# Kernel tuning notes

Measured on AMD Instinct MI355X. Metric: run time of the kernel, lower is better.

Reference implementation:

```python
import jax, jax.numpy as jnp
import numpy as np

K = 3          # kernel size
PAD = 1        # padding


def _conv2d(x, w, b):
    # plain 3x3 conv, stride 1, pad 1, NCHW / OIHW
    out = jax.lax.conv_general_dilated(
        x, w, window_strides=(1, 1), padding=((PAD, PAD), (PAD, PAD)),
        dimension_numbers=('NCHW', 'OIHW', 'NCHW'))
    return out + b[None, :, None, None]


def _deform_conv2d(x, offsets, w, b):
    # torchvision deform_conv2d semantics (stride=1, dilation=1, no mask)
    B, C, H, W = x.shape
    K2 = K * K
    off = offsets.reshape(B, K2, 2, H, W)
    dy, dx = off[:, :, 0], off[:, :, 1]              # [B,K2,H,W], (y,x) order
    ki, kj = jnp.meshgrid(jnp.arange(K), jnp.arange(K), indexing='ij')
    ki = ki.reshape(K2).astype(x.dtype)
    kj = kj.reshape(K2).astype(x.dtype)
    base_y = (jnp.arange(H, dtype=x.dtype)[None, :, None] - PAD + ki[:, None, None])  # [K2,H,1]
    base_x = (jnp.arange(W, dtype=x.dtype)[None, None, :] - PAD + kj[:, None, None])  # [K2,1,W]
    py = base_y[None] + dy                            # [B,K2,H,W] sampling rows
    px = base_x[None] + dx                            # [B,K2,H,W] sampling cols

    y0 = jnp.floor(py); x0 = jnp.floor(px)
    y1 = y0 + 1.0;      x1 = x0 + 1.0
    wy1 = py - y0; wy0 = 1.0 - wy1
    wx1 = px - x0; wx0 = 1.0 - wx1

    def corner(yc, xc, wgt):
        valid = ((yc >= 0) & (yc <= H - 1) & (xc >= 0) & (xc <= W - 1))
        iy = jnp.clip(yc, 0, H - 1).astype(jnp.int32)
        ix = jnp.clip(xc, 0, W - 1).astype(jnp.int32)
        # per-batch gather: x[b][:, iy[b], ix[b]] -> [C,K2,H,W]
        vals = jax.vmap(lambda xb, iyb, ixb: xb[:, iyb, ixb])(x, iy, ix)
        return vals * (wgt * valid.astype(x.dtype))[:, None]  # [B,C,K2,H,W]

    sampled = (corner(y0, x0, wy0 * wx0) + corner(y0, x1, wy0 * wx1)
               + corner(y1, x0, wy1 * wx0) + corner(y1, x1, wy1 * wx1))
    out = jnp.einsum('bckhw,ock->bohw', sampled, w.reshape(w.shape[0], C, K2))
    return out + b[None, :, None, None]


def setup_inputs() -> dict:
    key = jax.random.key(0)
    ks = jax.random.split(key, 6)
    B, C, O, H, W = 4, 256, 256, 64, 64
    x = jax.random.normal(ks[0], (B, C, H, W), dtype=jnp.float32)
    y = jax.random.normal(ks[1], (B, C, H, W), dtype=jnp.float32)
    # offset conv predicts 2*K*K offset channels; small init keeps offsets a few px
    offset_w = jax.random.normal(ks[2], (2 * K * K, C, K, K), dtype=jnp.float32) * 0.01
    offset_b = jax.random.normal(ks[3], (2 * K * K,), dtype=jnp.float32) * 0.01
    deform_w = jax.random.normal(ks[4], (O, C, K, K), dtype=jnp.float32) * (1.0 / np.sqrt(C * K * K))
    deform_b = jax.random.normal(ks[5], (O,), dtype=jnp.float32) * 0.01
    return {"x": x, "y": y, "offset_w": offset_w, "offset_b": offset_b,
            "deform_w": deform_w, "deform_b": deform_b}


def reference(x, y, offset_w, offset_b, deform_w, deform_b):
    offsets = _conv2d(y, offset_w, offset_b)          # [B, 2*K*K, H, W]
    return _deform_conv2d(x, offsets, deform_w, deform_b)
```

## Files before the change

### kernel.cpp

```cpp
#include <hip/hip_runtime.h>
#include <hip/hip_bf16.h>
#include <stdint.h>


typedef __bf16 bf16x8 __attribute__((ext_vector_type(8)));
typedef float  f32x4  __attribute__((ext_vector_type(4)));

__device__ __forceinline__ unsigned short f2bfu(float f) {
    union { float f; unsigned u; } v; v.f = f;
    return (unsigned short)((v.u + 0x8000u) >> 16);
}
__device__ __forceinline__ float lo16(unsigned u) {
    union { unsigned u; float f; } v; v.u = u << 16; return v.f;
}
__device__ __forceinline__ float hi16(unsigned u) {
    union { unsigned u; float f; } v; v.u = u & 0xFFFF0000u; return v.f;
}
__device__ __forceinline__ unsigned cvtpk_bf16(float lo, float hi) {
    unsigned r;
    asm("v_cvt_pk_bf16_f32 %0, %1, %2" : "=v"(r) : "v"(lo), "v"(hi));
    return r;
}
__device__ __forceinline__ unsigned blend2(unsigned u0, unsigned u1, unsigned u2, unsigned u3,
                                           float4 w) {
    float lo = w.x * lo16(u0) + w.y * lo16(u1) + w.z * lo16(u2) + w.w * lo16(u3);
    float hi = w.x * hi16(u0) + w.y * hi16(u1) + w.z * hi16(u2) + w.w * hi16(u3);
    return cvtpk_bf16(lo, hi);
}

__global__ __launch_bounds__(256) void prep_kernel(
    const float* __restrict__ x, const float* __restrict__ y,
    const float* __restrict__ ow, const float* __restrict__ dw,
    unsigned short* __restrict__ xT, unsigned short* __restrict__ yT,
    unsigned short* __restrict__ Wp2, unsigned short* __restrict__ Bo)
{
    __shared__ float tile[64 * 69];
    int blk = blockIdx.x;
    int t = threadIdx.x;
    if (blk < 2048) {
        const float* src = x; unsigned short* dst = xT;
        if (blk >= 1024) { src = y; dst = yT; blk -= 1024; }
        int cq = blk & 3;
        int bh = blk >> 2;
        int w4 = t & 15, cl0 = t >> 4;
        const float* s = src + ((size_t)(bh >> 6) * 256 + cq * 64) * 4096 + (size_t)(bh & 63) * 64;
#pragma unroll
        for (int p = 0; p < 4; ++p) {
            int cl = p * 16 + cl0;
            float4 v = *(const float4*)&s[(size_t)cl * 4096 + w4 * 4];
            tile[(w4 * 4 + 0) * 69 + cl] = v.x;
            tile[(w4 * 4 + 1) * 69 + cl] = v.y;
            tile[(w4 * 4 + 2) * 69 + cl] = v.z;
            tile[(w4 * 4 + 3) * 69 + cl] = v.w;
        }
        __syncthreads();
        unsigned short* d = dst + (size_t)bh * 16384 + cq * 64;
#pragma unroll
        for (int p = 0; p < 4; ++p) {
            int w = p * 16 + cl0;
            float4 v = *(const float4*)&tile[w * 69 + w4 * 4];
            ushort4 r = make_ushort4(f2bfu(v.x), f2bfu(v.y), f2bfu(v.z), f2bfu(v.w));
            *(ushort4*)&d[w * 256 + w4 * 4] = r;
        }
    } else if (blk < 2336) {
        int tid = (blk - 2048) * 256 + t;
        int q8 = tid >> 8;
        int o  = tid & 255;
        int k0 = q8 * 8;
        int tap = k0 >> 8, c0 = k0 & 255;
        const float* s = dw + o * 2304 + c0 * 9 + tap;
        ushort4 r0 = make_ushort4(f2bfu(s[0]), f2bfu(s[9]), f2bfu(s[18]), f2bfu(s[27]));
        ushort4 r1 = make_ushort4(f2bfu(s[36]), f2bfu(s[45]), f2bfu(s[54]), f2bfu(s[63]));
        *(ushort4*)&Wp2[tid * 8 + 0] = r0;
        *(ushort4*)&Wp2[tid * 8 + 4] = r1;
    } else {
        int idx = (blk - 2336) * 256 + t;
        int j = idx & 7;
        int n = (idx >> 3) & 31;
        int lq = (idx >> 8) & 3;
        int kg = idx >> 10;
        int k = kg * 32 + lq * 8 + j;
        int tap = k >> 8, c = k & 255;
        float v = (n < 18) ? ow[n * 2304 + c * 9 + tap] : 0.f;
        Bo[idx] = f2bfu(v);
    }
}


__device__ __forceinline__ void prod_half(int tap, int bp, int gr, int c0,
                                          const unsigned short* __restrict__ xtb,
                                          const float4* __restrict__ pw_lds,
                                          const int4* __restrict__ pi_lds,
                                          unsigned short* __restrict__ buf)
{
    uint4 ga[2][4]; float4 gw[2];
#pragma unroll
    for (int it = 0; it < 2; ++it) {
        int pos = bp + it * 16;
        gw[it] = pw_lds[tap * 64 + pos];
        int4 p = pi_lds[tap * 64 + pos];
        ga[it][0] = *(const uint4*)&xtb[p.x + c0];
        ga[it][1] = *(const uint4*)&xtb[p.y + c0];
        ga[it][2] = *(const uint4*)&xtb[p.z + c0];
        ga[it][3] = *(const uint4*)&xtb[p.w + c0];
    }
#pragma unroll
    for (int it = 0; it < 2; ++it) {
        int pos = bp + it * 16;
        uint4 res;
        res.x = blend2(ga[it][0].x, ga[it][1].x, ga[it][2].x, ga[it][3].x, gw[it]);
        res.y = blend2(ga[it][0].y, ga[it][1].y, ga[it][2].y, ga[it][3].y, gw[it]);
        res.z = blend2(ga[it][0].z, ga[it][1].z, ga[it][2].z, ga[it][3].z, gw[it]);
        res.w = blend2(ga[it][0].w, ga[it][1].w, ga[it][2].w, ga[it][3].w, gw[it]);
        *(uint4*)&buf[pos * 256 + (gr ^ (pos & 7)) * 8] = res;
    }
}

__device__ __forceinline__ void prod_tap(int tap, int p0, int gr, int c0,
                                         const unsigned short* __restrict__ xtb,
                                         const float4* __restrict__ pw_lds,
                                         const int4* __restrict__ pi_lds,
                                         unsigned short* __restrict__ buf)
{
    prod_half(tap, p0,      gr, c0, xtb, pw_lds, pi_lds, buf);
    prod_half(tap, p0 + 32, gr, c0, xtb, pw_lds, pi_lds, buf);
}

__device__ __forceinline__ void cons_tap(f32x4 (&acc)[4][2],
                                         const unsigned short* __restrict__ Ab,
                                         const unsigned short* __restrict__ Wp2,
                                         int tap, int lq, int ln, int ns)
{
#pragma unroll
    for (int kc = 0; kc < 8; ++kc) {
        int gbase = kc * 4 + lq;
        bf16x8 af[4];
#pragma unroll
        for (int ms = 0; ms < 4; ++ms) {
            int row = ms * 16 + ln;
            af[ms] = *(const bf16x8*)&Ab[row * 256 + (gbase ^ (row & 7)) * 8];
        }
        int kg = tap * 8 + kc;
        bf16x8 bfr[2];
#pragma unroll
        for (int nt = 0; nt < 2; ++nt)
            bfr[nt] = *(const bf16x8*)&Wp2[((kg * 4 + lq) * 256 + ns * 32 + nt * 16 + ln) * 8];
        __builtin_amdgcn_s_setprio(1);
#pragma unroll
        for (int ms = 0; ms < 4; ++ms)
#pragma unroll
            for (int nt = 0; nt < 2; ++nt)
                acc[ms][nt] = __builtin_amdgcn_mfma_f32_16x16x32_bf16(af[ms], bfr[nt], acc[ms][nt], 0, 0, 0);
        __builtin_amdgcn_s_setprio(0);
    }
}

__global__ __launch_bounds__(1024) void deform_kernel(
    const unsigned short* __restrict__ xT,
    const unsigned short* __restrict__ yT,
    const unsigned short* __restrict__ Wp2,
    const unsigned short* __restrict__ Bo,
    const float* __restrict__ ob,
    const float* __restrict__ db,
    float* __restrict__ out)
{
    __shared__ __align__(16) unsigned char smem[149504];
    unsigned short* Abase = (unsigned short*)smem;
    float*  red = (float*)smem;
    float4* pw_lds = (float4*)(smem + 131072);
    int4*   pi_lds = (int4*)(smem + 131072 + 9216);

    int blk = blockIdx.x;
    int lb = (blk & 7) * 32 + (blk >> 3);
    int b = lb >> 6, h = lb & 63;
    int t = threadIdx.x;
    int wv = t >> 6, lane = t & 63;
    int ln = lane & 15, lq = lane >> 4;

    const unsigned short* xtb = xT + (size_t)b * (64 * 64 * 256);

    {
        int kq = wv >> 1, mh = wv & 1;
        f32x4 oacc[2][2];
#pragma unroll
        for (int m16 = 0; m16 < 2; ++m16)
#pragma unroll
            for (int nt = 0; nt < 2; ++nt)
                oacc[m16][nt] = (f32x4){0.f, 0.f, 0.f, 0.f};
        for (int u = kq * 9; u < kq * 9 + 9; ++u) {
            int tap = u >> 3, kc = u & 7;
            int ki = tap / 3, kj = tap - ki * 3;
            int hr = h + ki - 1;
            bf16x8 b0 = *(const bf16x8*)&Bo[(tap * 8 + kc) * 1024 + lq * 256 + ln * 8];
            bf16x8 b1 = *(const bf16x8*)&Bo[(tap * 8 + kc) * 1024 + lq * 256 + (16 + ln) * 8];
#pragma unroll
            for (int m16 = 0; m16 < 2; ++m16) {
                int wr = mh * 32 + m16 * 16 + ln + kj - 1;
                bf16x8 af = (bf16x8)(__bf16)0.0f;
                if (hr >= 0 && hr < 64 && wr >= 0 && wr < 64)
                    af = *(const bf16x8*)&yT[((size_t)(b * 64 + hr) * 64 + wr) * 256 + kc * 32 + lq * 8];
                oacc[m16][0] = __builtin_amdgcn_mfma_f32_16x16x32_bf16(af, b0, oacc[m16][0], 0, 0, 0);
                oacc[m16][1] = __builtin_amdgcn_mfma_f32_16x16x32_bf16(af, b1, oacc[m16][1], 0, 0, 0);
            }
        }
        float* rz = red + (size_t)(kq * 2 + mh) * 1056;
#pragma unroll
        for (int m16 = 0; m16 < 2; ++m16)
#pragma unroll
            for (int nt = 0; nt < 2; ++nt) {
                int o_l = nt * 16 + ln;
#pragma unroll
                for (int r = 0; r < 4; ++r)
                    rz[o_l * 33 + m16 * 16 + lq * 4 + r] = oacc[m16][nt][r];
            }
    }
    __syncthreads();
    if (t < 576) {
        int tap = t >> 6, pos = t & 63;
        int mh_p = pos >> 5, pl = pos & 31;
        float dy = ob[2 * tap], dx = ob[2 * tap + 1];
#pragma unroll
        for (int kq = 0; kq < 8; ++kq) {
            const float* rz = red + (size_t)(kq * 2 + mh_p) * 1056;
            dy += rz[(2 * tap) * 33 + pl];
            dx += rz[(2 * tap + 1) * 33 + pl];
        }
        int ki = tap / 3, kj = tap - ki * 3;
        float py = (float)(h - 1 + ki) + dy;
        float px = (float)(pos - 1 + kj) + dx;
        float y0 = floorf(py), x0 = floorf(px);
        float wy1 = py - y0, wx1 = px - x0;
        float wy0 = 1.f - wy1, wx0 = 1.f - wx1;
        float y1 = y0 + 1.f, x1 = x0 + 1.f;
        float vy0 = (y0 >= 0.f && y0 <= 63.f) ? 1.f : 0.f;
        float vy1 = (y1 >= 0.f && y1 <= 63.f) ? 1.f : 0.f;
        float vx0 = (x0 >= 0.f && x0 <= 63.f) ? 1.f : 0.f;
        float vx1 = (x1 >= 0.f && x1 <= 63.f) ? 1.f : 0.f;
        int iy0 = (int)fminf(fmaxf(y0, 0.f), 63.f);
        int iy1 = (int)fminf(fmaxf(y1, 0.f), 63.f);
        int ix0 = (int)fminf(fmaxf(x0, 0.f), 63.f);
        int ix1 = (int)fminf(fmaxf(x1, 0.f), 63.f);
        pw_lds[t] = make_float4(wy0 * wx0 * vy0 * vx0, wy0 * wx1 * vy0 * vx1,
                                wy1 * wx0 * vy1 * vx0, wy1 * wx1 * vy1 * vx1);
        pi_lds[t] = make_int4((iy0 * 64 + ix0) * 256, (iy0 * 64 + ix1) * 256,
                              (iy1 * 64 + ix0) * 256, (iy1 * 64 + ix1) * 256);
    }
    __syncthreads();

    int ns = wv & 7;
    bool isProd = (wv >= 8);
    int gr = t & 31, c0 = gr * 8;
    int p0 = (t >> 5) & 15;

    f32x4 acc[4][2];
#pragma unroll
    for (int ms = 0; ms < 4; ++ms)
#pragma unroll
        for (int nt = 0; nt < 2; ++nt)
            acc[ms][nt] = (f32x4){0.f, 0.f, 0.f, 0.f};

    if (isProd) {
        prod_tap(0, p0, gr, c0, xtb, pw_lds, pi_lds, Abase + 0 * 16384);
        prod_tap(1, p0, gr, c0, xtb, pw_lds, pi_lds, Abase + 1 * 16384);
    }
    __syncthreads();

    for (int tap = 0; tap < 9; ++tap) {
        if (isProd) {
            if (tap < 7)
                prod_tap(tap + 2, p0, gr, c0, xtb, pw_lds, pi_lds,
                         Abase + ((tap + 2) & 3) * 16384);
        } else {
            cons_tap(acc, Abase + (tap & 3) * 16384, Wp2, tap, lq, ln, ns);
        }
        __syncthreads();
    }

    if (!isProd) {
#pragma unroll
        for (int ms = 0; ms < 4; ++ms)
#pragma unroll
            for (int nt = 0; nt < 2; ++nt) {
                int o = ns * 32 + nt * 16 + ln;
                float bias = db[o];
                f32x4 a = acc[ms][nt];
                float4 st = make_float4(a[0] + bias, a[1] + bias,
                                        a[2] + bias, a[3] + bias);
                *(float4*)&out[((size_t)(b * 256 + o)) * 4096 + h * 64 + ms * 16 + lq * 4] = st;
            }
    }
}

extern "C" void kernel_launch(void* const* d_in, const int* in_sizes, int n_in,
                              void* d_out, int out_size, void* d_ws, size_t ws_size,
                              hipStream_t stream) {
    const float* x  = (const float*)d_in[0];
    const float* y  = (const float*)d_in[1];
    const float* ow = (const float*)d_in[2];
    const float* ob = (const float*)d_in[3];
    const float* dw = (const float*)d_in[4];
    const float* db = (const float*)d_in[5];
    float* out = (float*)d_out;

    char* ws = (char*)d_ws;
    unsigned short* xT  = (unsigned short*)(ws);
    unsigned short* yT  = (unsigned short*)(ws + 8388608);
    unsigned short* Wp2 = (unsigned short*)(ws + 16777216);
    unsigned short* Bo  = (unsigned short*)(ws + 16777216 + 1179648);

    hipLaunchKernelGGL(prep_kernel, dim3(2624), dim3(256), 0, stream,
                       x, y, ow, dw, xT, yT, Wp2, Bo);
    hipLaunchKernelGGL(deform_kernel, dim3(256), dim3(1024), 0, stream,
                       xT, yT, Wp2, Bo, ob, db, out);
}
```

Measured before the change: 138.6 us.

## Split offset conv into separate kernel and halve deform tile per block

```diff
diff --git a/kernel.cpp b/kernel.cpp
--- a/kernel.cpp
+++ b/kernel.cpp
@@ -86,98 +86,19 @@
     }
 }
 
-
-__device__ __forceinline__ void prod_half(int tap, int bp, int gr, int c0,
-                                          const unsigned short* __restrict__ xtb,
-                                          const float4* __restrict__ pw_lds,
-                                          const int4* __restrict__ pi_lds,
-                                          unsigned short* __restrict__ buf)
-{
-    uint4 ga[2][4]; float4 gw[2];
-#pragma unroll
-    for (int it = 0; it < 2; ++it) {
-        int pos = bp + it * 16;
-        gw[it] = pw_lds[tap * 64 + pos];
-        int4 p = pi_lds[tap * 64 + pos];
-        ga[it][0] = *(const uint4*)&xtb[p.x + c0];
-        ga[it][1] = *(const uint4*)&xtb[p.y + c0];
-        ga[it][2] = *(const uint4*)&xtb[p.z + c0];
-        ga[it][3] = *(const uint4*)&xtb[p.w + c0];
-    }
-#pragma unroll
-    for (int it = 0; it < 2; ++it) {
-        int pos = bp + it * 16;
-        uint4 res;
-        res.x = blend2(ga[it][0].x, ga[it][1].x, ga[it][2].x, ga[it][3].x, gw[it]);
-        res.y = blend2(ga[it][0].y, ga[it][1].y, ga[it][2].y, ga[it][3].y, gw[it]);
-        res.z = blend2(ga[it][0].z, ga[it][1].z, ga[it][2].z, ga[it][3].z, gw[it]);
-        res.w = blend2(ga[it][0].w, ga[it][1].w, ga[it][2].w, ga[it][3].w, gw[it]);
-        *(uint4*)&buf[pos * 256 + (gr ^ (pos & 7)) * 8] = res;
-    }
-}
-
-__device__ __forceinline__ void prod_tap(int tap, int p0, int gr, int c0,
-                                         const unsigned short* __restrict__ xtb,
-                                         const float4* __restrict__ pw_lds,
-                                         const int4* __restrict__ pi_lds,
-                                         unsigned short* __restrict__ buf)
-{
-    prod_half(tap, p0,      gr, c0, xtb, pw_lds, pi_lds, buf);
-    prod_half(tap, p0 + 32, gr, c0, xtb, pw_lds, pi_lds, buf);
-}
-
-__device__ __forceinline__ void cons_tap(f32x4 (&acc)[4][2],
-                                         const unsigned short* __restrict__ Ab,
-                                         const unsigned short* __restrict__ Wp2,
-                                         int tap, int lq, int ln, int ns)
-{
-#pragma unroll
-    for (int kc = 0; kc < 8; ++kc) {
-        int gbase = kc * 4 + lq;
-        bf16x8 af[4];
-#pragma unroll
-        for (int ms = 0; ms < 4; ++ms) {
-            int row = ms * 16 + ln;
-            af[ms] = *(const bf16x8*)&Ab[row * 256 + (gbase ^ (row & 7)) * 8];
-        }
-        int kg = tap * 8 + kc;
-        bf16x8 bfr[2];
-#pragma unroll
-        for (int nt = 0; nt < 2; ++nt)
-            bfr[nt] = *(const bf16x8*)&Wp2[((kg * 4 + lq) * 256 + ns * 32 + nt * 16 + ln) * 8];
-        __builtin_amdgcn_s_setprio(1);
-#pragma unroll
-        for (int ms = 0; ms < 4; ++ms)
-#pragma unroll
-            for (int nt = 0; nt < 2; ++nt)
-                acc[ms][nt] = __builtin_amdgcn_mfma_f32_16x16x32_bf16(af[ms], bfr[nt], acc[ms][nt], 0, 0, 0);
-        __builtin_amdgcn_s_setprio(0);
-    }
-}
-
-__global__ __launch_bounds__(1024) void deform_kernel(
-    const unsigned short* __restrict__ xT,
+__global__ __launch_bounds__(1024) void offs_kernel(
     const unsigned short* __restrict__ yT,
-    const unsigned short* __restrict__ Wp2,
     const unsigned short* __restrict__ Bo,
     const float* __restrict__ ob,
-    const float* __restrict__ db,
-    float* __restrict__ out)
+    float* __restrict__ pypx)
 {
-    __shared__ __align__(16) unsigned char smem[149504];
-    unsigned short* Abase = (unsigned short*)smem;
-    float*  red = (float*)smem;
-    float4* pw_lds = (float4*)(smem + 131072);
-    int4*   pi_lds = (int4*)(smem + 131072 + 9216);
-
+    __shared__ float red[16 * 1056];
     int blk = blockIdx.x;
     int lb = (blk & 7) * 32 + (blk >> 3);
     int b = lb >> 6, h = lb & 63;
     int t = threadIdx.x;
     int wv = t >> 6, lane = t & 63;
     int ln = lane & 15, lq = lane >> 4;
-
-    const unsigned short* xtb = xT + (size_t)b * (64 * 64 * 256);
 
     {
         int kq = wv >> 1, mh = wv & 1;
@@ -228,6 +149,42 @@
         int ki = tap / 3, kj = tap - ki * 3;
         float py = (float)(h - 1 + ki) + dy;
         float px = (float)(pos - 1 + kj) + dx;
+        size_t o = (((size_t)(b * 64 + h) * 9 + tap) * 64 + pos) * 2;
+        pypx[o]     = py;
+        pypx[o + 1] = px;
+    }
+}
+
+__global__ __launch_bounds__(512) void deform_kernel(
+    const unsigned short* __restrict__ xT,
+    const unsigned short* __restrict__ Wp2,
+    const float* __restrict__ pypx,
+    const float* __restrict__ db,
+    float* __restrict__ out)
+{
+    __shared__ __align__(16) unsigned char smem[41984];
+    unsigned short* Ab0 = (unsigned short*)smem;
+    unsigned short* Ab1 = (unsigned short*)(smem + 16384);
+    float4* pw_lds = (float4*)(smem + 32768);
+    int4*   pi_lds = (int4*)(smem + 32768 + 4608);
+
+    int blk = blockIdx.x;
+    int lb = (blk & 7) * 64 + (blk >> 3);
+    int bh = lb >> 1, mh = lb & 1;
+    int b = bh >> 6, h = bh & 63;
+    int t = threadIdx.x;
+    int wv = t >> 6, lane = t & 63;
+    int ln = lane & 15, lq = lane >> 4;
+    int ns = wv;
+    int gr = t & 31, c0 = gr * 8;
+
+    const unsigned short* xtb = xT + (size_t)b * (64 * 64 * 256);
+
+    if (t < 288) {
+        int tap = t >> 5, pl = t & 31;
+        int w = mh * 32 + pl;
+        size_t o = (((size_t)bh * 9 + tap) * 64 + w) * 2;
+        float py = pypx[o], px = pypx[o + 1];
         float y0 = floorf(py), x0 = floorf(px);
         float wy1 = py - y0, wx1 = px - x0;
         float wy0 = 1.f - wy1, wx0 = 1.f - wx1;
@@ -247,48 +204,79 @@
     }
     __syncthreads();
 
-    int ns = wv & 7;
-    bool isProd = (wv >= 8);
-    int gr = t & 31, c0 = gr * 8;
-    int p0 = (t >> 5) & 15;
-
-    f32x4 acc[4][2];
-#pragma unroll
-    for (int ms = 0; ms < 4; ++ms)
+    f32x4 acc[2][2];
+#pragma unroll
+    for (int ms = 0; ms < 2; ++ms)
 #pragma unroll
         for (int nt = 0; nt < 2; ++nt)
             acc[ms][nt] = (f32x4){0.f, 0.f, 0.f, 0.f};
 
-    if (isProd) {
-        prod_tap(0, p0, gr, c0, xtb, pw_lds, pi_lds, Abase + 0 * 16384);
-        prod_tap(1, p0, gr, c0, xtb, pw_lds, pi_lds, Abase + 1 * 16384);
-    }
+    auto stage = [&](int tap, unsigned short* buf) {
+        uint4 ga[2][4]; float4 gw[2];
+#pragma unroll
+        for (int it = 0; it < 2; ++it) {
+            int pos = (t >> 5) + it * 16;
+            gw[it] = pw_lds[tap * 32 + pos];
+            int4 p = pi_lds[tap * 32 + pos];
+            ga[it][0] = *(const uint4*)&xtb[p.x + c0];
+            ga[it][1] = *(const uint4*)&xtb[p.y + c0];
+            ga[it][2] = *(const uint4*)&xtb[p.z + c0];
+            ga[it][3] = *(const uint4*)&xtb[p.w + c0];
+        }
+#pragma unroll
+        for (int it = 0; it < 2; ++it) {
+            int pos = (t >> 5) + it * 16;
+            uint4 res;
+            res.x = blend2(ga[it][0].x, ga[it][1].x, ga[it][2].x, ga[it][3].x, gw[it]);
+            res.y = blend2(ga[it][0].y, ga[it][1].y, ga[it][2].y, ga[it][3].y, gw[it]);
+            res.z = blend2(ga[it][0].z, ga[it][1].z, ga[it][2].z, ga[it][3].z, gw[it]);
+            res.w = blend2(ga[it][0].w, ga[it][1].w, ga[it][2].w, ga[it][3].w, gw[it]);
+            *(uint4*)&buf[pos * 256 + (gr ^ (pos & 7)) * 8] = res;
+        }
+    };
+
+    stage(0, Ab0);
     __syncthreads();
 
     for (int tap = 0; tap < 9; ++tap) {
-        if (isProd) {
-            if (tap < 7)
-                prod_tap(tap + 2, p0, gr, c0, xtb, pw_lds, pi_lds,
-                         Abase + ((tap + 2) & 3) * 16384);
-        } else {
-            cons_tap(acc, Abase + (tap & 3) * 16384, Wp2, tap, lq, ln, ns);
-        }
+        if (tap < 8)
+            stage(tap + 1, ((tap + 1) & 1) ? Ab1 : Ab0);
+        const unsigned short* Ab = (tap & 1) ? Ab1 : Ab0;
+        __builtin_amdgcn_s_setprio(1);
+#pragma unroll
+        for (int kc = 0; kc < 8; ++kc) {
+            int gbase = kc * 4 + lq;
+            bf16x8 af[2];
+#pragma unroll
+            for (int ms = 0; ms < 2; ++ms) {
+                int row = ms * 16 + ln;
+                af[ms] = *(const bf16x8*)&Ab[row * 256 + (gbase ^ (row & 7)) * 8];
+            }
+            int kg = tap * 8 + kc;
+            bf16x8 bfr[2];
+#pragma unroll
+            for (int nt = 0; nt < 2; ++nt)
+                bfr[nt] = *(const bf16x8*)&Wp2[((kg * 4 + lq) * 256 + ns * 32 + nt * 16 + ln) * 8];
+#pragma unroll
+            for (int ms = 0; ms < 2; ++ms)
+#pragma unroll
+                for (int nt = 0; nt < 2; ++nt)
+                    acc[ms][nt] = __builtin_amdgcn_mfma_f32_16x16x32_bf16(af[ms], bfr[nt], acc[ms][nt], 0, 0, 0);
+        }
+        __builtin_amdgcn_s_setprio(0);
         __syncthreads();
     }
 
-    if (!isProd) {
-#pragma unroll
-        for (int ms = 0; ms < 4; ++ms)
-#pragma unroll
-            for (int nt = 0; nt < 2; ++nt) {
-                int o = ns * 32 + nt * 16 + ln;
-                float bias = db[o];
-                f32x4 a = acc[ms][nt];
-                float4 st = make_float4(a[0] + bias, a[1] + bias,
-                                        a[2] + bias, a[3] + bias);
-                *(float4*)&out[((size_t)(b * 256 + o)) * 4096 + h * 64 + ms * 16 + lq * 4] = st;
-            }
-    }
+#pragma unroll
+    for (int ms = 0; ms < 2; ++ms)
+#pragma unroll
+        for (int nt = 0; nt < 2; ++nt) {
+            int o = ns * 32 + nt * 16 + ln;
+            float bias = db[o];
+            f32x4 a = acc[ms][nt];
+            float4 st = make_float4(a[0] + bias, a[1] + bias, a[2] + bias, a[3] + bias);
+            *(float4*)&out[((size_t)(b * 256 + o)) * 4096 + h * 64 + mh * 32 + ms * 16 + lq * 4] = st;
+        }
 }
 
 extern "C" void kernel_launch(void* const* d_in, const int* in_sizes, int n_in,
@@ -303,13 +291,16 @@
     float* out = (float*)d_out;
 
     char* ws = (char*)d_ws;
-    unsigned short* xT  = (unsigned short*)(ws);
-    unsigned short* yT  = (unsigned short*)(ws + 8388608);
-    unsigned short* Wp2 = (unsigned short*)(ws + 16777216);
-    unsigned short* Bo  = (unsigned short*)(ws + 16777216 + 1179648);
+    unsigned short* xT   = (unsigned short*)(ws);
+    unsigned short* yT   = (unsigned short*)(ws + 8388608);
+    unsigned short* Wp2  = (unsigned short*)(ws + 16777216);
+    unsigned short* Bo   = (unsigned short*)(ws + 16777216 + 1179648);
+    float*          pypx = (float*)(ws + 18104320);
 
     hipLaunchKernelGGL(prep_kernel, dim3(2624), dim3(256), 0, stream,
                        x, y, ow, dw, xT, yT, Wp2, Bo);
-    hipLaunchKernelGGL(deform_kernel, dim3(256), dim3(1024), 0, stream,
-                       xT, yT, Wp2, Bo, ob, db, out);
-}
+    hipLaunchKernelGGL(offs_kernel, dim3(256), dim3(1024), 0, stream,
+                       yT, Bo, ob, pypx);
+    hipLaunchKernelGGL(deform_kernel, dim3(512), dim3(512), 0, stream,
+                       xT, Wp2, pypx, db, out);
+}
```

After: 141.4 us. 1.02x slower.
